# Kernel tuning notes

Measured on AMD Instinct MI355X. Metric: run time of the kernel, lower is better.

The kernel has to match this reference:

```python
import jax, jax.numpy as jnp
import numpy as np

N, NFEAT, NHID = 10000, 128, 64


def _gc(x, adj, W, b):
    # GraphConvolution: adj @ (x @ W) + b
    return adj @ (x @ W) + b


def _fwd(x, adj, Wg0, bg0, Wg1, bg1, Wt0, bt0, Wt1, bt1,
         W000, b000, W001, b001, W100, b100, W101, b101,
         Wo0, bo0, Wo1, bo1, Wpp, bpp, Wpp2, bpp2, a, t):
    H = Wg0.shape[1]
    # outcome GCN stack (n_in=2), dropout is eval no-op
    rep_o = jax.nn.relu(_gc(x, adj, Wg0, bg0))
    rep_o = jax.nn.relu(_gc(rep_o, adj, Wg1, bg1))
    # treatment GCN stack
    rep_t = jax.nn.relu(_gc(x, adj, Wt0, bt0))
    rep_t = jax.nn.relu(_gc(rep_t, adj, Wt1, bt1))

    rep_cat = jnp.concatenate([rep_o, rep_t], axis=1)  # [N, 2H]
    # edge score(i,j) = [rep_cat_i ; rep_cat_j] @ a  =  s_src_i + s_dst_j
    s_src = rep_cat @ a[:2 * H, 0]   # [N]
    s_dst = rep_cat @ a[2 * H:, 0]   # [N]
    scores = s_src[:, None] + s_dst[None, :]          # [N, N]
    # only nonzero adj entries get a score; rest remain 0 (index_put into zeros)
    att = jnp.where(adj != 0, scores, jnp.zeros((), scores.dtype))
    att = jax.nn.softmax(att, axis=1)                 # full dense row softmax

    rep_out = att @ rep_t + rep_o                     # [N, H]

    treatment = jax.nn.sigmoid((rep_t @ Wpp + bpp) @ Wpp2 + bpp2)  # [N, 2]

    rep0 = rep_out
    rep1 = rep_out
    y00 = jax.nn.relu(rep0 @ W000 + b000)
    y10 = jax.nn.relu(rep1 @ W100 + b100)
    y00 = jax.nn.relu(y00 @ W001 + b001)
    y10 = jax.nn.relu(y10 @ W101 + b101)
    y0 = (y00 @ Wo0 + bo0).reshape(-1)
    y1 = (y10 @ Wo1 + bo1).reshape(-1)
    y = jnp.where(t > 0, y1, y0)
    return (y, rep_out, treatment)


def setup_inputs() -> dict:
    key = jax.random.key(0)
    ks = jax.random.split(key, 32)
    H = NHID
    x = jax.random.normal(ks[0], (N, NFEAT), dtype=jnp.float32)
    u = jax.random.uniform(ks[1], (N, N), dtype=jnp.float32)
    adj = jnp.where(u < 0.002, u, jnp.zeros((), jnp.float32))
    t = jax.random.randint(ks[2], (N,), 0, 2, dtype=jnp.int32)

    def lin(k, fi, fo):
        s = 1.0 / np.sqrt(fi)
        kw, kb = jax.random.split(k)
        return (jax.random.uniform(kw, (fi, fo), jnp.float32, -s, s),
                jax.random.uniform(kb, (fo,), jnp.float32, -s, s))

    Wg0, bg0 = lin(ks[3], NFEAT, H)
    Wg1, bg1 = lin(ks[4], H, H)
    Wt0, bt0 = lin(ks[5], NFEAT, H)
    Wt1, bt1 = lin(ks[6], H, H)
    W000, b000 = lin(ks[7], H, H)
    W001, b001 = lin(ks[8], H, H)
    W100, b100 = lin(ks[9], H, H)
    W101, b101 = lin(ks[10], H, H)
    Wo0, bo0 = lin(ks[11], H, 1)
    Wo1, bo1 = lin(ks[12], H, 1)
    Wpp, bpp = lin(ks[13], H, H)
    Wpp2, bpp2 = lin(ks[14], H, 2)
    # torch init is xavier with gain=0 (all zeros); use small random for a
    # meaningful correctness baseline
    a = jax.random.normal(ks[15], (4 * H, 1), dtype=jnp.float32) * 0.1
    return dict(x=x, adj=adj, t=t,
                Wg0=Wg0, bg0=bg0, Wg1=Wg1, bg1=bg1,
                Wt0=Wt0, bt0=bt0, Wt1=Wt1, bt1=bt1,
                W000=W000, b000=b000, W001=W001, b001=b001,
                W100=W100, b100=b100, W101=W101, b101=b101,
                Wo0=Wo0, bo0=bo0, Wo1=Wo1, bo1=bo1,
                Wpp=Wpp, bpp=bpp, Wpp2=Wpp2, bpp2=bpp2, a=a)


def reference(x, adj, t, Wg0, bg0, Wg1, bg1, Wt0, bt0, Wt1, bt1,
              W000, b000, W001, b001, W100, b100, W101, b101,
              Wo0, bo0, Wo1, bo1, Wpp, bpp, Wpp2, bpp2, a):
    return _fwd(x, adj, Wg0, bg0, Wg1, bg1, Wt0, bt0, Wt1, bt1,
                W000, b000, W001, b001, W100, b100, W101, b101,
                Wo0, bo0, Wo1, bo1, Wpp, bpp, Wpp2, bpp2, a, t)
```

## Files before the change

### kernel.cpp

```cpp
#include <hip/hip_runtime.h>
#include <hip/hip_bf16.h>

#define N_NODES 10000
#define ROW4    2500
#define CAP     64
#define SPAR_BLOCKS 2500
#define TOTAL_K1    3750

typedef float fx4 __attribute__((ext_vector_type(4)));

#define OFF_CNT     0
#define OFF_COLSUM  10000
#define OFF_SSRC    10064
#define OFF_SDST    20064
#define OFF_PAIRS   30064
#define OFF_B1      1310064
#define OFF_B2      1950064
#define OFF_B3      2590064
#define OFF_B4      3230064

__device__ __forceinline__ float wave_sum(float v) {
    #pragma unroll
    for (int off = 32; off >= 1; off >>= 1) v += __shfl_xor(v, off, 64);
    return v;
}
__device__ __forceinline__ float wave_max(float v) {
    #pragma unroll
    for (int off = 32; off >= 1; off >>= 1) v = fmaxf(v, __shfl_xor(v, off, 64));
    return v;
}

__global__ void k1_fused(const fx4* __restrict__ adj4, const float* __restrict__ x,
                         const float* __restrict__ Wg0, const float* __restrict__ Wt0,
                         int* __restrict__ cnt, float2* __restrict__ pairs,
                         float* __restrict__ colsum,
                         float* __restrict__ P, float* __restrict__ Q) {
    __shared__ float xs[8 * 128];
    int tid = threadIdx.x;
    if (blockIdx.x < SPAR_BLOCKS) {
        int lane = tid & 63, w = tid >> 6;
        int row = blockIdx.x * 4 + w;
        if (blockIdx.x == 0 && tid < 64) colsum[tid] = 0.0f;
        const fx4* rp = adj4 + (size_t)row * ROW4;
        size_t base = (size_t)row * CAP;
        int count = 0;
        for (int it = 0; it < 40; it += 8) {
            fx4 v[8];
            #pragma unroll
            for (int j = 0; j < 8; ++j) {
                int idx = (it + j) * 64 + lane;
                v[j] = (fx4){0.f, 0.f, 0.f, 0.f};
                if (idx < ROW4) v[j] = __builtin_nontemporal_load(rp + idx);
            }
            #pragma unroll
            for (int j = 0; j < 8; ++j) {
                int idx = (it + j) * 64 + lane;
                float vv[4] = {v[j].x, v[j].y, v[j].z, v[j].w};
                bool any = (vv[0] != 0.f) | (vv[1] != 0.f) | (vv[2] != 0.f) | (vv[3] != 0.f);
                if (__ballot(any)) {
                    #pragma unroll
                    for (int l = 0; l < 4; ++l) {
                        unsigned long long b = __ballot(vv[l] != 0.f);
                        if (b) {
                            int pre = __popcll(b & ((1ull << lane) - 1ull));
                            if (vv[l] != 0.f) {
                                int pos = count + pre;
                                if (pos < CAP)
                                    pairs[base + pos] =
                                        make_float2(__int_as_float(idx * 4 + l), vv[l]);
                            }
                            count += (int)__popcll(b);
                        }
                    }
                }
            }
        }
        if (lane == 0) cnt[row] = min(count, CAP);
    } else {
        int row0 = (blockIdx.x - SPAR_BLOCKS) * 8;
        ((float4*)xs)[tid] = ((const float4*)(x + (size_t)row0 * 128))[tid];
        __syncthreads();
        int sub = tid >> 6, f = tid & 63;
        #pragma unroll
        for (int g = 0; g < 2; ++g) {
            const float* xr = xs + (g * 4 + sub) * 128;
            float aP = 0.0f, aQ = 0.0f;
            #pragma unroll 8
            for (int k = 0; k < 128; k += 4) {
                float4 xv = *(const float4*)(xr + k);
                aP += xv.x * Wg0[(k + 0) * 64 + f] + xv.y * Wg0[(k + 1) * 64 + f]
                    + xv.z * Wg0[(k + 2) * 64 + f] + xv.w * Wg0[(k + 3) * 64 + f];
                aQ += xv.x * Wt0[(k + 0) * 64 + f] + xv.y * Wt0[(k + 1) * 64 + f]
                    + xv.z * Wt0[(k + 2) * 64 + f] + xv.w * Wt0[(k + 3) * 64 + f];
            }
            P[(size_t)(row0 + g * 4 + sub) * 64 + f] = aP;
            Q[(size_t)(row0 + g * 4 + sub) * 64 + f] = aQ;
        }
    }
}

__global__ void k2_agg_gemm(const int* __restrict__ cnt, const float2* __restrict__ pairs,
                            const float* __restrict__ P, const float* __restrict__ Q,
                            const float* __restrict__ bg0, const float* __restrict__ bt0,
                            const float* __restrict__ Wg1, const float* __restrict__ Wt1,
                            float* __restrict__ P2, float* __restrict__ Q2) {
    __shared__ float ra[8 * 64], rb[8 * 64];
    int tid = threadIdx.x, row0 = blockIdx.x * 8, sub = tid >> 6, f = tid & 63;
    float bo = bg0[f], bt = bt0[f];
    #pragma unroll
    for (int g = 0; g < 2; ++g) {
        int lr = g * 4 + sub, row = row0 + lr;
        int c = min(cnt[row], CAP);
        float2 pr = make_float2(0.f, 0.f);
        if (f < c) pr = pairs[(size_t)row * CAP + f];
        int c_l = __float_as_int(pr.x); float v_l = pr.y;
        float a0 = 0.f, a1 = 0.f, b0 = 0.f, b1 = 0.f;
        for (int p = 0; p < c; p += 8) {
            #pragma unroll
            for (int j = 0; j < 8; j += 2) {
                float vv0 = __shfl(v_l, p + j, 64);     int cc0 = __shfl(c_l, p + j, 64);
                float vv1 = __shfl(v_l, p + j + 1, 64); int cc1 = __shfl(c_l, p + j + 1, 64);
                a0 += vv0 * P[(size_t)cc0 * 64 + f];
                b0 += vv0 * Q[(size_t)cc0 * 64 + f];
                a1 += vv1 * P[(size_t)cc1 * 64 + f];
                b1 += vv1 * Q[(size_t)cc1 * 64 + f];
            }
        }
        ra[lr * 64 + f] = fmaxf(a0 + a1 + bo, 0.0f);
        rb[lr * 64 + f] = fmaxf(b0 + b1 + bt, 0.0f);
    }
    __syncthreads();
    #pragma unroll
    for (int g = 0; g < 2; ++g) {
        int lr = g * 4 + sub, row = row0 + lr;
        const float* rra = ra + lr * 64;
        const float* rrb = rb + lr * 64;
        float aA = 0.f, aB = 0.f;
        #pragma unroll 8
        for (int k = 0; k < 64; k += 4) {
            float4 va = *(const float4*)(rra + k);
            float4 vb = *(const float4*)(rrb + k);
            aA += va.x * Wg1[(k + 0) * 64 + f] + va.y * Wg1[(k + 1) * 64 + f]
                + va.z * Wg1[(k + 2) * 64 + f] + va.w * Wg1[(k + 3) * 64 + f];
            aB += vb.x * Wt1[(k + 0) * 64 + f] + vb.y * Wt1[(k + 1) * 64 + f]
                + vb.z * Wt1[(k + 2) * 64 + f] + vb.w * Wt1[(k + 3) * 64 + f];
        }
        P2[(size_t)row * 64 + f] = aA;
        Q2[(size_t)row * 64 + f] = aB;
    }
}

__global__ void k3_agg_score(const int* __restrict__ cnt, const float2* __restrict__ pairs,
                             const float* __restrict__ P2, const float* __restrict__ Q2,
                             const float* __restrict__ bg1, const float* __restrict__ bt1,
                             const float* __restrict__ a,
                             const float* __restrict__ Wpp, const float* __restrict__ bpp,
                             const float* __restrict__ Wpp2, const float* __restrict__ bpp2,
                             float* __restrict__ rep_o, float* __restrict__ rep_t,
                             float* __restrict__ s_src, float* __restrict__ s_dst,
                             float* __restrict__ colsum, float* __restrict__ out_trt) {
    __shared__ float rts[8 * 64];
    int tid = threadIdx.x, row0 = blockIdx.x * 8, sub = tid >> 6, f = tid & 63;
    float bo = bg1[f], bt = bt1[f];
    float a0c = a[f], a1c = a[64 + f], a2c = a[128 + f], a3c = a[192 + f];
    #pragma unroll
    for (int g = 0; g < 2; ++g) {
        int lr = g * 4 + sub, row = row0 + lr;
        int c = min(cnt[row], CAP);
        float2 pr = make_float2(0.f, 0.f);
        if (f < c) pr = pairs[(size_t)row * CAP + f];
        int c_l = __float_as_int(pr.x); float v_l = pr.y;
        float a0 = 0.f, a1 = 0.f, b0 = 0.f, b1 = 0.f;
        for (int p = 0; p < c; p += 8) {
            #pragma unroll
            for (int j = 0; j < 8; j += 2) {
                float vv0 = __shfl(v_l, p + j, 64);     int cc0 = __shfl(c_l, p + j, 64);
                float vv1 = __shfl(v_l, p + j + 1, 64); int cc1 = __shfl(c_l, p + j + 1, 64);
                a0 += vv0 * P2[(size_t)cc0 * 64 + f];
                b0 += vv0 * Q2[(size_t)cc0 * 64 + f];
                a1 += vv1 * P2[(size_t)cc1 * 64 + f];
                b1 += vv1 * Q2[(size_t)cc1 * 64 + f];
            }
        }
        float vo = fmaxf(a0 + a1 + bo, 0.0f);
        float vt = fmaxf(b0 + b1 + bt, 0.0f);
        rep_o[(size_t)row * 64 + f] = vo;
        rep_t[(size_t)row * 64 + f] = vt;
        rts[lr * 64 + f] = vt;
        float ps = wave_sum(vo * a0c + vt * a1c);
        float pd = wave_sum(vo * a2c + vt * a3c);
        if (f == 0) { s_src[row] = ps; s_dst[row] = pd; }
    }
    __syncthreads();
    if (sub == 0) {
        float cs = 0.0f;
        #pragma unroll
        for (int lr = 0; lr < 8; ++lr) cs += rts[lr * 64 + f];
        atomicAdd(&colsum[f], cs);
    }
    float bp = bpp[f], w20 = Wpp2[f * 2 + 0], w21 = Wpp2[f * 2 + 1];
    #pragma unroll
    for (int g = 0; g < 2; ++g) {
        int lr = g * 4 + sub, row = row0 + lr;
        const float* rr = rts + lr * 64;
        float u = bp;
        #pragma unroll 8
        for (int k = 0; k < 64; k += 4) {
            float4 rv = *(const float4*)(rr + k);
            u += rv.x * Wpp[(k + 0) * 64 + f] + rv.y * Wpp[(k + 1) * 64 + f]
               + rv.z * Wpp[(k + 2) * 64 + f] + rv.w * Wpp[(k + 3) * 64 + f];
        }
        float p0 = wave_sum(u * w20);
        float p1 = wave_sum(u * w21);
        if (f == 0) {
            out_trt[(size_t)row * 2 + 0] = 1.0f / (1.0f + expf(-(p0 + bpp2[0])));
            out_trt[(size_t)row * 2 + 1] = 1.0f / (1.0f + expf(-(p1 + bpp2[1])));
        }
    }
}

__global__ void k4_attn_heads(const int* __restrict__ cnt, const float2* __restrict__ pairs,
                              const float* __restrict__ s_src, const float* __restrict__ s_dst,
                              const float* __restrict__ colsum,
                              const float* __restrict__ rep_o, const float* __restrict__ rep_t,
                              const float* __restrict__ W000, const float* __restrict__ b000,
                              const float* __restrict__ W001, const float* __restrict__ b001,
                              const float* __restrict__ W100, const float* __restrict__ b100,
                              const float* __restrict__ W101, const float* __restrict__ b101,
                              const float* __restrict__ Wo0, const float* __restrict__ bo0,
                              const float* __restrict__ Wo1, const float* __restrict__ bo1,
                              const int* __restrict__ t,
                              float* __restrict__ out_y, float* __restrict__ out_rep) {
    __shared__ float reps[8 * 64], u0s[8 * 64], u1s[8 * 64];
    int tid = threadIdx.x, row0 = blockIdx.x * 8, sub = tid >> 6, f = tid & 63;
    float csf = colsum[f];
    #pragma unroll
    for (int g = 0; g < 2; ++g) {
        int lr = g * 4 + sub, row = row0 + lr;
        int c = min(cnt[row], CAP);
        float ssrc = s_src[row];
        int   col_l = (f < c) ? __float_as_int(pairs[(size_t)row * CAP + f].x) : 0;
        float s_l   = (f < c) ? ssrc + s_dst[col_l] : -1e30f;
        float m = fmaxf(wave_max(s_l), 0.0f);
        float e_l = (f < c) ? expf(s_l - m) : 0.0f;
        float em = expf(-m);
        float Z = wave_sum(e_l) + (float)(N_NODES - c) * em;
        float g_l = (f < c) ? (e_l - em) : 0.0f;
        float a0 = 0.f, a1 = 0.f, a2 = 0.f, a3 = 0.f;
        for (int p = 0; p < c; p += 8) {
            #pragma unroll
            for (int j = 0; j < 8; j += 4) {
                float g0 = __shfl(g_l, p + j + 0, 64); int c0 = __shfl(col_l, p + j + 0, 64);
                float g1 = __shfl(g_l, p + j + 1, 64); int c1 = __shfl(col_l, p + j + 1, 64);
                float g2 = __shfl(g_l, p + j + 2, 64); int c2 = __shfl(col_l, p + j + 2, 64);
                float g3 = __shfl(g_l, p + j + 3, 64); int c3 = __shfl(col_l, p + j + 3, 64);
                a0 += g0 * rep_t[(size_t)c0 * 64 + f];
                a1 += g1 * rep_t[(size_t)c1 * 64 + f];
                a2 += g2 * rep_t[(size_t)c2 * 64 + f];
                a3 += g3 * rep_t[(size_t)c3 * 64 + f];
            }
        }
        float outv = ((a0 + a1 + a2 + a3) + em * csf) / Z + rep_o[(size_t)row * 64 + f];
        out_rep[(size_t)row * 64 + f] = outv;
        reps[lr * 64 + f] = outv;
    }
    __syncthreads();
    float bA = b000[f], bB = b100[f];
    #pragma unroll
    for (int g = 0; g < 2; ++g) {
        int lr = g * 4 + sub;
        const float* rr = reps + lr * 64;
        float u0 = bA, u1 = bB;
        #pragma unroll 8
        for (int k = 0; k < 64; k += 4) {
            float4 rv = *(const float4*)(rr + k);
            u0 += rv.x * W000[(k + 0) * 64 + f] + rv.y * W000[(k + 1) * 64 + f]
                + rv.z * W000[(k + 2) * 64 + f] + rv.w * W000[(k + 3) * 64 + f];
            u1 += rv.x * W100[(k + 0) * 64 + f] + rv.y * W100[(k + 1) * 64 + f]
                + rv.z * W100[(k + 2) * 64 + f] + rv.w * W100[(k + 3) * 64 + f];
        }
        u0s[lr * 64 + f] = fmaxf(u0, 0.0f);
        u1s[lr * 64 + f] = fmaxf(u1, 0.0f);
    }
    __syncthreads();
    float bC = b001[f], bD = b101[f], wo0 = Wo0[f], wo1 = Wo1[f];
    #pragma unroll
    for (int g = 0; g < 2; ++g) {
        int lr = g * 4 + sub, row = row0 + lr;
        const float* r0 = u0s + lr * 64;
        const float* r1 = u1s + lr * 64;
        float v0 = bC, v1 = bD;
        #pragma unroll 8
        for (int k = 0; k < 64; k += 4) {
            float4 q0 = *(const float4*)(r0 + k);
            float4 q1 = *(const float4*)(r1 + k);
            v0 += q0.x * W001[(k + 0) * 64 + f] + q0.y * W001[(k + 1) * 64 + f]
                + q0.z * W001[(k + 2) * 64 + f] + q0.w * W001[(k + 3) * 64 + f];
            v1 += q1.x * W101[(k + 0) * 64 + f] + q1.y * W101[(k + 1) * 64 + f]
                + q1.z * W101[(k + 2) * 64 + f] + q1.w * W101[(k + 3) * 64 + f];
        }
        float y0 = wave_sum(fmaxf(v0, 0.0f) * wo0);
        float y1 = wave_sum(fmaxf(v1, 0.0f) * wo1);
        if (f == 0)
            out_y[row] = (t[row] > 0) ? (y1 + bo1[0]) : (y0 + bo0[0]);
    }
}


extern "C" void kernel_launch(void* const* d_in, const int* in_sizes, int n_in,
                              void* d_out, int out_size, void* d_ws, size_t ws_size,
                              hipStream_t stream) {
    const float* x    = (const float*)d_in[0];
    const float* adj  = (const float*)d_in[1];
    const int*   t    = (const int*)d_in[2];
    const float* Wg0  = (const float*)d_in[3];
    const float* bg0  = (const float*)d_in[4];
    const float* Wg1  = (const float*)d_in[5];
    const float* bg1  = (const float*)d_in[6];
    const float* Wt0  = (const float*)d_in[7];
    const float* bt0  = (const float*)d_in[8];
    const float* Wt1  = (const float*)d_in[9];
    const float* bt1  = (const float*)d_in[10];
    const float* W000 = (const float*)d_in[11];
    const float* b000 = (const float*)d_in[12];
    const float* W001 = (const float*)d_in[13];
    const float* b001 = (const float*)d_in[14];
    const float* W100 = (const float*)d_in[15];
    const float* b100 = (const float*)d_in[16];
    const float* W101 = (const float*)d_in[17];
    const float* b101 = (const float*)d_in[18];
    const float* Wo0  = (const float*)d_in[19];
    const float* bo0  = (const float*)d_in[20];
    const float* Wo1  = (const float*)d_in[21];
    const float* bo1  = (const float*)d_in[22];
    const float* Wpp  = (const float*)d_in[23];
    const float* bpp  = (const float*)d_in[24];
    const float* Wpp2 = (const float*)d_in[25];
    const float* bpp2 = (const float*)d_in[26];
    const float* a    = (const float*)d_in[27];

    float* ws = (float*)d_ws;
    int*    cnt    = (int*)(ws + OFF_CNT);
    float*  colsum = ws + OFF_COLSUM;
    float*  s_src  = ws + OFF_SSRC;
    float*  s_dst  = ws + OFF_SDST;
    float2* pairs  = (float2*)(ws + OFF_PAIRS);
    float*  B1     = ws + OFF_B1;
    float*  B2     = ws + OFF_B2;
    float*  B3     = ws + OFF_B3;
    float*  B4     = ws + OFF_B4;

    float* out_y   = (float*)d_out;
    float* out_rep = (float*)d_out + N_NODES;
    float* out_trt = (float*)d_out + N_NODES + N_NODES * 64;

    k1_fused<<<TOTAL_K1, 256, 0, stream>>>((const fx4*)adj, x, Wg0, Wt0,
                                           cnt, pairs, colsum, B1, B2);
    k2_agg_gemm<<<1250, 256, 0, stream>>>(cnt, pairs, B1, B2, bg0, bt0, Wg1, Wt1, B3, B4);
    k3_agg_score<<<1250, 256, 0, stream>>>(cnt, pairs, B3, B4, bg1, bt1, a,
                                           Wpp, bpp, Wpp2, bpp2,
                                           B1, B2, s_src, s_dst, colsum, out_trt);
    k4_attn_heads<<<1250, 256, 0, stream>>>(cnt, pairs, s_src, s_dst, colsum, B1, B2,
                                            W000, b000, W001, b001,
                                            W100, b100, W101, b101,
                                            Wo0, bo0, Wo1, bo1, t, out_y, out_rep);
}
```

Measured before the change: 655.7 us.

## Reassociate first GCN layer to aggregate x before dense weight GEMMs

```diff
diff --git a/kernel.cpp b/kernel.cpp
--- a/kernel.cpp
+++ b/kernel.cpp
@@ -4,8 +4,6 @@
 #define N_NODES 10000
 #define ROW4    2500
 #define CAP     64
-#define SPAR_BLOCKS 2500
-#define TOTAL_K1    3750
 
 typedef float fx4 __attribute__((ext_vector_type(4)));
 
@@ -14,8 +12,9 @@
 #define OFF_SSRC    10064
 #define OFF_SDST    20064
 #define OFF_PAIRS   30064
-#define OFF_B1      1310064
-#define OFF_B2      1950064
+#define OFF_AX      1310064
+#define OFF_REPO    1310064
+#define OFF_REPT    1950064
 #define OFF_B3      2590064
 #define OFF_B4      3230064
 
@@ -30,104 +29,93 @@
     return v;
 }
 
-__global__ void k1_fused(const fx4* __restrict__ adj4, const float* __restrict__ x,
-                         const float* __restrict__ Wg0, const float* __restrict__ Wt0,
-                         int* __restrict__ cnt, float2* __restrict__ pairs,
-                         float* __restrict__ colsum,
-                         float* __restrict__ P, float* __restrict__ Q) {
-    __shared__ float xs[8 * 128];
+__global__ void k1_sparsify_ax(const fx4* __restrict__ adj4, const float2* __restrict__ x2,
+                               int* __restrict__ cnt, float2* __restrict__ pairs,
+                               float* __restrict__ colsum, float2* __restrict__ Ax2) {
     int tid = threadIdx.x;
-    if (blockIdx.x < SPAR_BLOCKS) {
-        int lane = tid & 63, w = tid >> 6;
-        int row = blockIdx.x * 4 + w;
-        if (blockIdx.x == 0 && tid < 64) colsum[tid] = 0.0f;
-        const fx4* rp = adj4 + (size_t)row * ROW4;
-        size_t base = (size_t)row * CAP;
-        int count = 0;
-        for (int it = 0; it < 40; it += 8) {
-            fx4 v[8];
-            #pragma unroll
-            for (int j = 0; j < 8; ++j) {
-                int idx = (it + j) * 64 + lane;
-                v[j] = (fx4){0.f, 0.f, 0.f, 0.f};
-                if (idx < ROW4) v[j] = __builtin_nontemporal_load(rp + idx);
-            }
-            #pragma unroll
-            for (int j = 0; j < 8; ++j) {
-                int idx = (it + j) * 64 + lane;
-                float vv[4] = {v[j].x, v[j].y, v[j].z, v[j].w};
-                bool any = (vv[0] != 0.f) | (vv[1] != 0.f) | (vv[2] != 0.f) | (vv[3] != 0.f);
-                if (__ballot(any)) {
-                    #pragma unroll
-                    for (int l = 0; l < 4; ++l) {
-                        unsigned long long b = __ballot(vv[l] != 0.f);
-                        if (b) {
-                            int pre = __popcll(b & ((1ull << lane) - 1ull));
-                            if (vv[l] != 0.f) {
-                                int pos = count + pre;
-                                if (pos < CAP)
-                                    pairs[base + pos] =
-                                        make_float2(__int_as_float(idx * 4 + l), vv[l]);
-                            }
-                            count += (int)__popcll(b);
+    int lane = tid & 63, w = tid >> 6;
+    int row = blockIdx.x * 4 + w;
+    if (blockIdx.x == 0 && tid < 64) colsum[tid] = 0.0f;
+    const fx4* rp = adj4 + (size_t)row * ROW4;
+    size_t base = (size_t)row * CAP;
+    int count = 0;
+    for (int it = 0; it < 40; it += 8) {
+        fx4 v[8];
+        #pragma unroll
+        for (int j = 0; j < 8; ++j) {
+            int idx = (it + j) * 64 + lane;
+            v[j] = (fx4){0.f, 0.f, 0.f, 0.f};
+            if (idx < ROW4) v[j] = __builtin_nontemporal_load(rp + idx);
+        }
+        #pragma unroll
+        for (int j = 0; j < 8; ++j) {
+            int idx = (it + j) * 64 + lane;
+            float vv[4] = {v[j].x, v[j].y, v[j].z, v[j].w};
+            bool any = (vv[0] != 0.f) | (vv[1] != 0.f) | (vv[2] != 0.f) | (vv[3] != 0.f);
+            if (__ballot(any)) {
+                #pragma unroll
+                for (int l = 0; l < 4; ++l) {
+                    unsigned long long b = __ballot(vv[l] != 0.f);
+                    if (b) {
+                        int pre = __popcll(b & ((1ull << lane) - 1ull));
+                        if (vv[l] != 0.f) {
+                            int pos = count + pre;
+                            if (pos < CAP)
+                                pairs[base + pos] =
+                                    make_float2(__int_as_float(idx * 4 + l), vv[l]);
                         }
+                        count += (int)__popcll(b);
                     }
                 }
             }
         }
-        if (lane == 0) cnt[row] = min(count, CAP);
-    } else {
-        int row0 = (blockIdx.x - SPAR_BLOCKS) * 8;
-        ((float4*)xs)[tid] = ((const float4*)(x + (size_t)row0 * 128))[tid];
-        __syncthreads();
-        int sub = tid >> 6, f = tid & 63;
+    }
+    int c = min(count, CAP);
+    if (lane == 0) cnt[row] = c;
+    float2 pr = make_float2(0.f, 0.f);
+    if (lane < c) pr = pairs[base + lane];
+    int c_l = __float_as_int(pr.x); float v_l = pr.y;
+    float ax0 = 0.f, ay0 = 0.f, ax1 = 0.f, ay1 = 0.f;
+    for (int p = 0; p < c; p += 4) {
         #pragma unroll
-        for (int g = 0; g < 2; ++g) {
-            const float* xr = xs + (g * 4 + sub) * 128;
-            float aP = 0.0f, aQ = 0.0f;
-            #pragma unroll 8
-            for (int k = 0; k < 128; k += 4) {
-                float4 xv = *(const float4*)(xr + k);
-                aP += xv.x * Wg0[(k + 0) * 64 + f] + xv.y * Wg0[(k + 1) * 64 + f]
-                    + xv.z * Wg0[(k + 2) * 64 + f] + xv.w * Wg0[(k + 3) * 64 + f];
-                aQ += xv.x * Wt0[(k + 0) * 64 + f] + xv.y * Wt0[(k + 1) * 64 + f]
-                    + xv.z * Wt0[(k + 2) * 64 + f] + xv.w * Wt0[(k + 3) * 64 + f];
-            }
-            P[(size_t)(row0 + g * 4 + sub) * 64 + f] = aP;
-            Q[(size_t)(row0 + g * 4 + sub) * 64 + f] = aQ;
-        }
-    }
-}
-
-__global__ void k2_agg_gemm(const int* __restrict__ cnt, const float2* __restrict__ pairs,
-                            const float* __restrict__ P, const float* __restrict__ Q,
-                            const float* __restrict__ bg0, const float* __restrict__ bt0,
-                            const float* __restrict__ Wg1, const float* __restrict__ Wt1,
-                            float* __restrict__ P2, float* __restrict__ Q2) {
+        for (int j = 0; j < 4; j += 2) {
+            float vv0 = __shfl(v_l, p + j, 64);     int cc0 = __shfl(c_l, p + j, 64);
+            float vv1 = __shfl(v_l, p + j + 1, 64); int cc1 = __shfl(c_l, p + j + 1, 64);
+            float2 xa = x2[(size_t)cc0 * 64 + lane];
+            float2 xb = x2[(size_t)cc1 * 64 + lane];
+            ax0 += vv0 * xa.x; ay0 += vv0 * xa.y;
+            ax1 += vv1 * xb.x; ay1 += vv1 * xb.y;
+        }
+    }
+    Ax2[(size_t)row * 64 + lane] = make_float2(ax0 + ax1, ay0 + ay1);
+}
+
+__global__ void k2_dense(const float* __restrict__ Ax,
+                         const float* __restrict__ Wg0, const float* __restrict__ bg0,
+                         const float* __restrict__ Wt0, const float* __restrict__ bt0,
+                         const float* __restrict__ Wg1, const float* __restrict__ Wt1,
+                         float* __restrict__ P2, float* __restrict__ Q2) {
+    __shared__ float xs[8 * 128];
     __shared__ float ra[8 * 64], rb[8 * 64];
     int tid = threadIdx.x, row0 = blockIdx.x * 8, sub = tid >> 6, f = tid & 63;
+    ((float4*)xs)[tid] = ((const float4*)(Ax + (size_t)row0 * 128))[tid];
+    __syncthreads();
     float bo = bg0[f], bt = bt0[f];
     #pragma unroll
     for (int g = 0; g < 2; ++g) {
-        int lr = g * 4 + sub, row = row0 + lr;
-        int c = min(cnt[row], CAP);
-        float2 pr = make_float2(0.f, 0.f);
-        if (f < c) pr = pairs[(size_t)row * CAP + f];
-        int c_l = __float_as_int(pr.x); float v_l = pr.y;
-        float a0 = 0.f, a1 = 0.f, b0 = 0.f, b1 = 0.f;
-        for (int p = 0; p < c; p += 8) {
-            #pragma unroll
-            for (int j = 0; j < 8; j += 2) {
-                float vv0 = __shfl(v_l, p + j, 64);     int cc0 = __shfl(c_l, p + j, 64);
-                float vv1 = __shfl(v_l, p + j + 1, 64); int cc1 = __shfl(c_l, p + j + 1, 64);
-                a0 += vv0 * P[(size_t)cc0 * 64 + f];
-                b0 += vv0 * Q[(size_t)cc0 * 64 + f];
-                a1 += vv1 * P[(size_t)cc1 * 64 + f];
-                b1 += vv1 * Q[(size_t)cc1 * 64 + f];
-            }
-        }
-        ra[lr * 64 + f] = fmaxf(a0 + a1 + bo, 0.0f);
-        rb[lr * 64 + f] = fmaxf(b0 + b1 + bt, 0.0f);
+        int lr = g * 4 + sub;
+        const float* xr = xs + lr * 128;
+        float aP = 0.0f, aQ = 0.0f;
+        #pragma unroll 8
+        for (int k = 0; k < 128; k += 4) {
+            float4 xv = *(const float4*)(xr + k);
+            aP += xv.x * Wg0[(k + 0) * 64 + f] + xv.y * Wg0[(k + 1) * 64 + f]
+                + xv.z * Wg0[(k + 2) * 64 + f] + xv.w * Wg0[(k + 3) * 64 + f];
+            aQ += xv.x * Wt0[(k + 0) * 64 + f] + xv.y * Wt0[(k + 1) * 64 + f]
+                + xv.z * Wt0[(k + 2) * 64 + f] + xv.w * Wt0[(k + 3) * 64 + f];
+        }
+        ra[lr * 64 + f] = fmaxf(aP + bo, 0.0f);
+        rb[lr * 64 + f] = fmaxf(aQ + bt, 0.0f);
     }
     __syncthreads();
     #pragma unroll
@@ -345,8 +333,9 @@
     float*  s_src  = ws + OFF_SSRC;
     float*  s_dst  = ws + OFF_SDST;
     float2* pairs  = (float2*)(ws + OFF_PAIRS);
-    float*  B1     = ws + OFF_B1;
-    float*  B2     = ws + OFF_B2;
+    float*  Ax     = ws + OFF_AX;
+    float*  rep_o  = ws + OFF_REPO;
+    float*  rep_t  = ws + OFF_REPT;
     float*  B3     = ws + OFF_B3;
     float*  B4     = ws + OFF_B4;
 
@@ -354,13 +343,13 @@
     float* out_rep = (float*)d_out + N_NODES;
     float* out_trt = (float*)d_out + N_NODES + N_NODES * 64;
 
-    k1_fused<<<TOTAL_K1, 256, 0, stream>>>((const fx4*)adj, x, Wg0, Wt0,
-                                           cnt, pairs, colsum, B1, B2);
-    k2_agg_gemm<<<1250, 256, 0, stream>>>(cnt, pairs, B1, B2, bg0, bt0, Wg1, Wt1, B3, B4);
+    k1_sparsify_ax<<<2500, 256, 0, stream>>>((const fx4*)adj, (const float2*)x,
+                                             cnt, pairs, colsum, (float2*)Ax);
+    k2_dense<<<1250, 256, 0, stream>>>(Ax, Wg0, bg0, Wt0, bt0, Wg1, Wt1, B3, B4);
     k3_agg_score<<<1250, 256, 0, stream>>>(cnt, pairs, B3, B4, bg1, bt1, a,
                                            Wpp, bpp, Wpp2, bpp2,
-                                           B1, B2, s_src, s_dst, colsum, out_trt);
-    k4_attn_heads<<<1250, 256, 0, stream>>>(cnt, pairs, s_src, s_dst, colsum, B1, B2,
+                                           rep_o, rep_t, s_src, s_dst, colsum, out_trt);
+    k4_attn_heads<<<1250, 256, 0, stream>>>(cnt, pairs, s_src, s_dst, colsum, rep_o, rep_t,
                                             W000, b000, W001, b001,
                                             W100, b100, W101, b101,
                                             Wo0, bo0, Wo1, bo1, t, out_y, out_rep);
```

Result: slower. 670.7 us (+2.3%).

## Stream adjacency rows through LDS with async global_load_lds double buffering

Applied to the files above, without the earlier changes.

```diff
diff --git a/kernel.cpp b/kernel.cpp
--- a/kernel.cpp
+++ b/kernel.cpp
@@ -6,8 +6,6 @@
 #define CAP     64
 #define SPAR_BLOCKS 2500
 #define TOTAL_K1    3750
-
-typedef float fx4 __attribute__((ext_vector_type(4)));
 
 #define OFF_CNT     0
 #define OFF_COLSUM  10000
@@ -30,44 +28,61 @@
     return v;
 }
 
-__global__ void k1_fused(const fx4* __restrict__ adj4, const float* __restrict__ x,
+__global__ void k1_fused(const float4* __restrict__ adj4, const float* __restrict__ x,
                          const float* __restrict__ Wg0, const float* __restrict__ Wt0,
                          int* __restrict__ cnt, float2* __restrict__ pairs,
                          float* __restrict__ colsum,
                          float* __restrict__ P, float* __restrict__ Q) {
-    __shared__ float xs[8 * 128];
+    __shared__ float4 stage[4][2][512];
     int tid = threadIdx.x;
     if (blockIdx.x < SPAR_BLOCKS) {
         int lane = tid & 63, w = tid >> 6;
         int row = blockIdx.x * 4 + w;
         if (blockIdx.x == 0 && tid < 64) colsum[tid] = 0.0f;
-        const fx4* rp = adj4 + (size_t)row * ROW4;
+        const float4* rp = adj4 + (size_t)row * ROW4;
         size_t base = (size_t)row * CAP;
         int count = 0;
-        for (int it = 0; it < 40; it += 8) {
-            fx4 v[8];
+
+        #define ISSUE_CHUNK(c, buf)                                                   \
+            _Pragma("unroll")                                                          \
+            for (int k = 0; k < 8; ++k) {                                              \
+                int idx4 = (c) * 512 + k * 64 + lane;                                  \
+                if (idx4 < ROW4)                                                       \
+                    __builtin_amdgcn_global_load_lds(                                  \
+                        (const __attribute__((address_space(1))) void*)(rp + idx4),    \
+                        (__attribute__((address_space(3))) void*)&stage[w][buf][k*64], \
+                        16, 0, 2 );                     \
+            }
+
+        ISSUE_CHUNK(0, 0)
+        for (int c = 0; c < 5; ++c) {
+            if (c + 1 < 5) {
+                ISSUE_CHUNK(c + 1, (c + 1) & 1)
+                asm volatile("s_waitcnt vmcnt(8)" ::: "memory");
+            } else {
+                asm volatile("s_waitcnt vmcnt(0)" ::: "memory");
+            }
+            int buf = c & 1;
             #pragma unroll
-            for (int j = 0; j < 8; ++j) {
-                int idx = (it + j) * 64 + lane;
-                v[j] = (fx4){0.f, 0.f, 0.f, 0.f};
-                if (idx < ROW4) v[j] = __builtin_nontemporal_load(rp + idx);
-            }
-            #pragma unroll
-            for (int j = 0; j < 8; ++j) {
-                int idx = (it + j) * 64 + lane;
-                float vv[4] = {v[j].x, v[j].y, v[j].z, v[j].w};
-                bool any = (vv[0] != 0.f) | (vv[1] != 0.f) | (vv[2] != 0.f) | (vv[3] != 0.f);
+            for (int k = 0; k < 8; ++k) {
+                int idx4 = c * 512 + k * 64 + lane;
+                float4 v = stage[w][buf][k * 64 + lane];
+                bool in = idx4 < ROW4;
+                float vv[4] = {v.x, v.y, v.z, v.w};
+                bool any = in && ((vv[0] != 0.f) | (vv[1] != 0.f) |
+                                  (vv[2] != 0.f) | (vv[3] != 0.f));
                 if (__ballot(any)) {
                     #pragma unroll
                     for (int l = 0; l < 4; ++l) {
-                        unsigned long long b = __ballot(vv[l] != 0.f);
+                        bool nz = in && (vv[l] != 0.f);
+                        unsigned long long b = __ballot(nz);
                         if (b) {
                             int pre = __popcll(b & ((1ull << lane) - 1ull));
-                            if (vv[l] != 0.f) {
+                            if (nz) {
                                 int pos = count + pre;
                                 if (pos < CAP)
                                     pairs[base + pos] =
-                                        make_float2(__int_as_float(idx * 4 + l), vv[l]);
+                                        make_float2(__int_as_float(idx4 * 4 + l), vv[l]);
                             }
                             count += (int)__popcll(b);
                         }
@@ -75,8 +90,10 @@
                 }
             }
         }
+        #undef ISSUE_CHUNK
         if (lane == 0) cnt[row] = min(count, CAP);
     } else {
+        float* xs = (float*)stage;
         int row0 = (blockIdx.x - SPAR_BLOCKS) * 8;
         ((float4*)xs)[tid] = ((const float4*)(x + (size_t)row0 * 128))[tid];
         __syncthreads();
@@ -354,7 +371,7 @@
     float* out_rep = (float*)d_out + N_NODES;
     float* out_trt = (float*)d_out + N_NODES + N_NODES * 64;
 
-    k1_fused<<<TOTAL_K1, 256, 0, stream>>>((const fx4*)adj, x, Wg0, Wt0,
+    k1_fused<<<TOTAL_K1, 256, 0, stream>>>((const float4*)adj, x, Wg0, Wt0,
                                            cnt, pairs, colsum, B1, B2);
     k2_agg_gemm<<<1250, 256, 0, stream>>>(cnt, pairs, B1, B2, bg0, bt0, Wg1, Wt1, B3, B4);
     k3_agg_score<<<1250, 256, 0, stream>>>(cnt, pairs, B3, B4, bg1, bt1, a,
```

After: 658.1 us. About the same (+0.4%).
